# Optimization experiments

Hardware: AMD Instinct MI355X
Metric: run time of the kernel (lower is better)

The kernel has to match this reference:

```python
import jax, jax.numpy as jnp
import numpy as np

B, T, C, H = 4, 1024, 1024, 16
HD = C // H
EPS = 1e-5


def _layernorm(x, w, b):
    mu = jnp.mean(x, axis=-1, keepdims=True)
    var = jnp.mean(jnp.square(x - mu), axis=-1, keepdims=True)
    return (x - mu) * jax.lax.rsqrt(var + EPS) * w + b


def setup_inputs() -> dict:
    key = jax.random.key(0)
    ks = jax.random.split(key, 10)
    s = 0.02
    return {
        "x": jax.random.normal(ks[0], (B, T, C), jnp.float32),
        "attention_mask": jnp.zeros((1, 1, T, T), jnp.float32),
        "ln1_w": jnp.ones((C,), jnp.float32),
        "ln1_b": jnp.zeros((C,), jnp.float32),
        "w_qkv": s * jax.random.normal(ks[1], (3 * C, C), jnp.float32),
        "b_qkv": jnp.zeros((3 * C,), jnp.float32),
        "w_o": s * jax.random.normal(ks[2], (C, C), jnp.float32),
        "b_o": jnp.zeros((C,), jnp.float32),
        "ln2_w": jnp.ones((C,), jnp.float32),
        "ln2_b": jnp.zeros((C,), jnp.float32),
        "w_fc": s * jax.random.normal(ks[3], (4 * C, C), jnp.float32),
        "b_fc": jnp.zeros((4 * C,), jnp.float32),
        "w_proj": s * jax.random.normal(ks[4], (C, 4 * C), jnp.float32),
        "b_proj": jnp.zeros((C,), jnp.float32),
    }


def reference(x, attention_mask, ln1_w, ln1_b, w_qkv, b_qkv, w_o, b_o,
              ln2_w, ln2_b, w_fc, b_fc, w_proj, b_proj):
    # --- self-attention on ln_1(x) ---
    h = _layernorm(x, ln1_w, ln1_b)
    qkv = h @ w_qkv.T + b_qkv                      # [B,T,3C]
    q, k, v = jnp.split(qkv, 3, axis=-1)
    q = q.reshape(B, T, H, HD).transpose(0, 2, 1, 3)  # [B,H,T,HD]
    k = k.reshape(B, T, H, HD).transpose(0, 2, 1, 3)
    v = v.reshape(B, T, H, HD).transpose(0, 2, 1, 3)
    att = jnp.einsum('bhqd,bhkd->bhqk', q, k) * (1.0 / np.sqrt(HD))
    att = att + attention_mask
    att_weights = jax.nn.softmax(att, axis=-1)     # [B,H,T,T]
    y = jnp.einsum('bhqk,bhkd->bhqd', att_weights, v)
    y = y.transpose(0, 2, 1, 3).reshape(B, T, C)
    y = y @ w_o.T + b_o
    x = x + y
    # --- MLP on ln_2(x), residual ---
    residual = x
    h2 = _layernorm(x, ln2_w, ln2_b)
    h2 = jax.nn.gelu(h2 @ w_fc.T + b_fc, approximate=False)
    h2 = h2 @ w_proj.T + b_proj
    x = residual + h2
    return (x, att_weights)
```

## Files before the change

kernel.cpp:

```cpp
#include <hip/hip_runtime.h>
#include <stdint.h>
#include <math.h>

typedef __attribute__((ext_vector_type(4))) float f32x4;
typedef __attribute__((ext_vector_type(8))) short s16x8;
typedef __attribute__((ext_vector_type(4))) unsigned short u16x4;
typedef __attribute__((ext_vector_type(8))) unsigned short u16x8;

__device__ __forceinline__ unsigned short f2b(float x) {
    union { float f; uint32_t u; } v; v.f = x;
    uint32_t r = v.u + 0x7FFFu + ((v.u >> 16) & 1u);
    return (unsigned short)(r >> 16);
}
__device__ __forceinline__ float b2f(unsigned short u) {
    union { uint32_t u; float f; } v; v.u = (uint32_t)u << 16;
    return v.f;
}

__device__ __forceinline__ void gload16(const unsigned short* g, unsigned short* l) {
    __builtin_amdgcn_global_load_lds(
        (const __attribute__((address_space(1))) unsigned int*)(const void*)g,
        (__attribute__((address_space(3))) unsigned int*)(void*)l,
        16, 0, 0);
}

__global__ __launch_bounds__(256) void cast4_kernel(
        const float* __restrict__ a, int na, const float* __restrict__ b, int nb,
        const float* __restrict__ c, int nc, const float* __restrict__ d, int nd,
        unsigned short* __restrict__ oa, unsigned short* __restrict__ ob,
        unsigned short* __restrict__ oc, unsigned short* __restrict__ od) {
    int i = blockIdx.x * 256 + threadIdx.x;
    const float* src; unsigned short* dst; int off;
    if (i < na)                { src = a; dst = oa; off = i; }
    else if (i < na+nb)        { src = b; dst = ob; off = i - na; }
    else if (i < na+nb+nc)     { src = c; dst = oc; off = i - na - nb; }
    else if (i < na+nb+nc+nd)  { src = d; dst = od; off = i - na - nb - nc; }
    else return;
    f32x4 v = ((const f32x4*)src)[off];
    u16x4 o;
    #pragma unroll
    for (int j = 0; j < 4; ++j) o[j] = f2b(v[j]);
    ((u16x4*)dst)[off] = o;
}

__global__ __launch_bounds__(256) void ln_kernel(const float* __restrict__ x,
                                                 const float* __restrict__ w,
                                                 const float* __restrict__ b,
                                                 unsigned short* __restrict__ out) {
    const long row = blockIdx.x;
    const int tid = threadIdx.x;
    f32x4 v = *(const f32x4*)(x + row * 1024 + tid * 4);
    float s  = v[0] + v[1] + v[2] + v[3];
    float sq = v[0]*v[0] + v[1]*v[1] + v[2]*v[2] + v[3]*v[3];
    #pragma unroll
    for (int off = 32; off; off >>= 1) {
        s  += __shfl_xor(s, off);
        sq += __shfl_xor(sq, off);
    }
    __shared__ float red[8];
    if ((tid & 63) == 0) { red[tid >> 6] = s; red[4 + (tid >> 6)] = sq; }
    __syncthreads();
    s  = red[0] + red[1] + red[2] + red[3];
    sq = red[4] + red[5] + red[6] + red[7];
    float mu  = s * (1.0f / 1024.0f);
    float var = sq * (1.0f / 1024.0f) - mu * mu;
    float rs  = rsqrtf(var + 1e-5f);
    f32x4 wv = *(const f32x4*)(w + tid * 4);
    f32x4 bv = *(const f32x4*)(b + tid * 4);
    u16x4 o;
    #pragma unroll
    for (int j = 0; j < 4; ++j) o[j] = f2b((v[j] - mu) * rs * wv[j] + bv[j]);
    *(u16x4*)(out + row * 1024 + tid * 4) = o;
}

__global__ __launch_bounds__(256) void inv_kernel(const float* __restrict__ psum,
                                                  float* __restrict__ invl) {
    const long r = blockIdx.x * 256 + threadIdx.x;
    const float* p = psum + (r << 4);
    f32x4 a = *(const f32x4*)p,       b = *(const f32x4*)(p + 4);
    f32x4 c = *(const f32x4*)(p + 8), d = *(const f32x4*)(p + 12);
    float s = (a[0]+a[1]+a[2]+a[3]) + (b[0]+b[1]+b[2]+b[3])
            + (c[0]+c[1]+c[2]+c[3]) + (d[0]+d[1]+d[2]+d[3]);
    invl[r] = 1.0f / s;
}

__global__ __launch_bounds__(256)
void pv_att(const unsigned short* __restrict__ E,
            const unsigned short* __restrict__ Vt,
            const float* __restrict__ invl,
            float* __restrict__ att,
            unsigned short* __restrict__ y) {
    __shared__ unsigned short ldsA[3][64 * 32];
    __shared__ unsigned short ldsB[3][64 * 32];
    const int tid = threadIdx.x, lane = tid & 63, wid = tid >> 6;
    const int wr = wid >> 1, wc = wid & 1;
    const int bh = blockIdx.y;
    const int q0 = blockIdx.x * 64;
    const int fr = lane & 15, fs = lane >> 4;

    const unsigned short* Ab = E + ((long)bh << 20) + (long)q0 * 1024;
    const unsigned short* Bb = Vt + ((long)bh << 16);

    const int e0  = wid * 512 + lane * 8;
    const int r0a = e0 >> 5, c0a = e0 & 31;
    const float il_a = invl[(bh << 10) + q0 + r0a];
    float* attRow = att + ((long)bh << 20) + (long)(q0 + r0a) * 1024 + c0a;

    f32x4 acc[2][2] = {};

#define PSTAGE(T, BUF)                                                        \
    {                                                                         \
        const int k0s = (T) << 5;                                             \
        gload16(Ab + k0s + (long)r0a * 1024 + c0a, &ldsA[BUF][wid * 512]);    \
        gload16(Bb + k0s + (long)r0a * 1024 + c0a, &ldsB[BUF][wid * 512]);    \
    }

    PSTAGE(0, 0);
    PSTAGE(1, 1);

    for (int t = 0; t < 32; ++t) {
        const int buf = t % 3;
        asm volatile("s_waitcnt vmcnt(4)" ::: "memory");
        __syncthreads();
        if (t + 2 < 32) PSTAGE(t + 2, (t + 2) % 3);

        {
            s16x8 ea = *(const s16x8*)&ldsA[buf][e0];
            f32x4 o0, o1;
            #pragma unroll
            for (int j = 0; j < 4; ++j) o0[j] = b2f((unsigned short)ea[j]) * il_a;
            #pragma unroll
            for (int j = 0; j < 4; ++j) o1[j] = b2f((unsigned short)ea[4 + j]) * il_a;
            *(f32x4*)(attRow + t * 32)     = o0;
            *(f32x4*)(attRow + t * 32 + 4) = o1;
        }

        s16x8 af[2], vb[2];
        #pragma unroll
        for (int m = 0; m < 2; ++m)
            af[m] = *(const s16x8*)&ldsA[buf][(wr * 32 + m * 16 + fr) * 32 + fs * 8];
        #pragma unroll
        for (int n = 0; n < 2; ++n)
            vb[n] = *(const s16x8*)&ldsB[buf][(wc * 32 + n * 16 + fr) * 32 + fs * 8];
        #pragma unroll
        for (int m = 0; m < 2; ++m)
            #pragma unroll
            for (int n = 0; n < 2; ++n)
                acc[m][n] = __builtin_amdgcn_mfma_f32_16x16x32_bf16(af[m], vb[n], acc[m][n], 0, 0, 0);
    }
#undef PSTAGE

    const int bb = bh >> 4, hh = bh & 15;
    #pragma unroll
    for (int m = 0; m < 2; ++m) {
        #pragma unroll
        for (int r = 0; r < 4; ++r) {
            const int trow = q0 + wr * 32 + m * 16 + fs * 4 + r;
            const float il = invl[(bh << 10) + trow];
            #pragma unroll
            for (int n = 0; n < 2; ++n) {
                const int c = hh * 64 + wc * 32 + n * 16 + fr;
                y[((long)(bb * 1024 + trow) << 10) + c] = f2b(acc[m][n][r] * il);
            }
        }
    }
}

template <int BM, int BN, int EPI>
__global__ __launch_bounds__(256)
void gemm_bt(const unsigned short* __restrict__ A,
             const unsigned short* __restrict__ Bm,
             int K, int lda, int ldb, int ldc,
             long sAz, long sBz,
             const float* __restrict__ bias,
             const float* __restrict__ resid,
             float* __restrict__ outF,
             unsigned short* __restrict__ outB) {
    constexpr int WM = BM / 2, WN = BN / 2;
    constexpr int FM = WM / 16, FN = WN / 16;
    constexpr int NTA = BM / 64, NTB = BN / 64;
    constexpr int LOADS = NTA + NTB;
    __shared__ unsigned short ldsA[3][BM * 32];
    __shared__ unsigned short ldsB[3][BN * 32];

    const int tid  = threadIdx.x;
    const int lane = tid & 63;
    const int wid  = tid >> 6;
    const int wr   = wid >> 1, wc = wid & 1;
    const int bz   = blockIdx.z;
    const int row0 = blockIdx.x * BM;
    const int col0 = blockIdx.y * BN;

    const unsigned short* Ab = A + (long)bz * sAz + (long)row0 * lda;
    const unsigned short* Bb = Bm + (long)bz * sBz + (long)col0 * ldb;

    const int nt = K >> 5;
    f32x4 acc[FM][FN] = {};
    const int fr = lane & 15;
    const int fk = (lane >> 4) * 8;

#define STAGE(T, BUF)                                                              \
    {                                                                              \
        const int k0s = (T) << 5;                                                  \
        _Pragma("unroll")                                                          \
        for (int i = 0; i < NTA; ++i) {                                            \
            int e = i * 2048 + wid * 512 + lane * 8;                               \
            gload16(Ab + k0s + (long)(e >> 5) * lda + (e & 31),                    \
                    &ldsA[BUF][i * 2048 + wid * 512]);                             \
        }                                                                          \
        _Pragma("unroll")                                                          \
        for (int i = 0; i < NTB; ++i) {                                            \
            int e = i * 2048 + wid * 512 + lane * 8;                               \
            gload16(Bb + k0s + (long)(e >> 5) * ldb + (e & 31),                    \
                    &ldsB[BUF][i * 2048 + wid * 512]);                             \
        }                                                                          \
    }

    STAGE(0, 0);
    if (nt > 1) STAGE(1, 1);

    for (int t = 0; t < nt; ++t) {
        const int buf = t % 3;
        if (t + 1 < nt) {
            if constexpr (LOADS == 2)      asm volatile("s_waitcnt vmcnt(2)" ::: "memory");
            else if constexpr (LOADS == 3) asm volatile("s_waitcnt vmcnt(3)" ::: "memory");
            else                           asm volatile("s_waitcnt vmcnt(4)" ::: "memory");
        } else {
            asm volatile("s_waitcnt vmcnt(0)" ::: "memory");
        }
        __syncthreads();
        if (t + 2 < nt) STAGE(t + 2, (t + 2) % 3);

        s16x8 af[FM], bfr[FN];
        #pragma unroll
        for (int m = 0; m < FM; ++m)
            af[m] = *(const s16x8*)&ldsA[buf][(wr * WM + m * 16 + fr) * 32 + fk];
        #pragma unroll
        for (int n = 0; n < FN; ++n)
            bfr[n] = *(const s16x8*)&ldsB[buf][(wc * WN + n * 16 + fr) * 32 + fk];
        #pragma unroll
        for (int m = 0; m < FM; ++m)
            #pragma unroll
            for (int n = 0; n < FN; ++n)
                acc[m][n] = __builtin_amdgcn_mfma_f32_16x16x32_bf16(af[m], bfr[n], acc[m][n], 0, 0, 0);
    }
#undef STAGE

    const int cj = lane & 15;
    const int r0 = (lane >> 4) * 4;

    if constexpr (EPI == 1) {
        #pragma unroll
        for (int m = 0; m < FM; ++m) {
            #pragma unroll
            for (int r = 0; r < 4; ++r) {
                const int grow = row0 + wr * WM + m * 16 + r0 + r;
                float rs = 0.0f;
                #pragma unroll
                for (int n = 0; n < FN; ++n) {
                    const int gcol = col0 + wc * WN + n * 16 + cj;
                    float e = __expf(acc[m][n][r] + resid[((long)grow << 10) + gcol]);
                    rs += e;
                    outB[((long)bz << 20) + ((long)grow << 10) + gcol] = f2b(e);
                }
                rs += __shfl_xor(rs, 1); rs += __shfl_xor(rs, 2);
                rs += __shfl_xor(rs, 4); rs += __shfl_xor(rs, 8);
                if (cj == 0)
                    outF[((((long)bz << 10) + grow) << 4) + blockIdx.y * 2 + wc] = rs;
            }
        }
    } else {
        #pragma unroll
        for (int m = 0; m < FM; ++m) {
            #pragma unroll
            for (int n = 0; n < FN; ++n) {
                #pragma unroll
                for (int r = 0; r < 4; ++r) {
                    const int grow = row0 + wr * WM + m * 16 + r0 + r;
                    const int gcol = col0 + wc * WN + n * 16 + cj;
                    float v = acc[m][n][r];
                    if constexpr (EPI == 0) {
                        v += bias[gcol];
                        const int bb = grow >> 10, t = grow & 1023;
                        const int seg = gcol >> 10, mm = gcol & 1023;
                        const int hh = mm >> 6, dd = mm & 63;
                        const long bh = bb * 16 + hh;
                        if (seg == 0)
                            outB[(bh << 16) + (t << 6) + dd] = f2b(v * 0.125f);
                        else if (seg == 1)
                            outB[4194304 + (bh << 16) + (t << 6) + dd] = f2b(v);
                        else
                            outB[8388608 + (bh << 16) + (dd << 10) + t] = f2b(v);
                    } else if constexpr (EPI == 3) {
                        const long idx = ((long)grow << 10) + gcol;
                        outF[idx] = v + bias[gcol] + resid[idx];
                    } else if constexpr (EPI == 4) {
                        float u = v + bias[gcol];
                        float g = 0.5f * u * (1.0f + erff(u * 0.70710678118f));
                        outB[(long)grow * ldc + gcol] = f2b(g);
                    }
                }
            }
        }
    }
}

extern "C" void kernel_launch(void* const* d_in, const int* in_sizes, int n_in,
                              void* d_out, int out_size, void* d_ws, size_t ws_size,
                              hipStream_t stream) {
    (void)in_sizes; (void)n_in; (void)out_size; (void)ws_size;
    const float* x     = (const float*)d_in[0];
    const float* mask  = (const float*)d_in[1];
    const float* ln1w  = (const float*)d_in[2];
    const float* ln1b  = (const float*)d_in[3];
    const float* wqkv  = (const float*)d_in[4];
    const float* bqkv  = (const float*)d_in[5];
    const float* wo    = (const float*)d_in[6];
    const float* bo    = (const float*)d_in[7];
    const float* ln2w  = (const float*)d_in[8];
    const float* ln2b  = (const float*)d_in[9];
    const float* wfc   = (const float*)d_in[10];
    const float* bfc   = (const float*)d_in[11];
    const float* wproj = (const float*)d_in[12];
    const float* bproj = (const float*)d_in[13];

    float* outx = (float*)d_out;
    float* att  = (float*)d_out + 4194304;

    char* ws = (char*)d_ws;
    unsigned short* h_bf     = (unsigned short*)ws;  ws += (size_t)8  << 20;
    unsigned short* wqkv_bf  = (unsigned short*)ws;  ws += (size_t)6  << 20;
    unsigned short* wo_bf    = (unsigned short*)ws;  ws += (size_t)2  << 20;
    unsigned short* wfc_bf   = (unsigned short*)ws;  ws += (size_t)8  << 20;
    unsigned short* wproj_bf = (unsigned short*)ws;  ws += (size_t)8  << 20;
    unsigned short* q_bf     = (unsigned short*)ws;  ws += (size_t)24 << 20;
    unsigned short* k_bf     = q_bf + 4194304;
    unsigned short* vT_bf    = q_bf + 8388608;
    unsigned short* e_b      = (unsigned short*)ws;  ws += (size_t)128 << 20;
    unsigned short* y_bf     = (unsigned short*)ws;  ws += (size_t)8  << 20;
    float*          x2       = (float*)ws;           ws += (size_t)16 << 20;
    unsigned short* gelu_bf  = (unsigned short*)ws;  ws += (size_t)32 << 20;
    float*          psum     = (float*)ws;           ws += (size_t)4  << 20;
    float*          invl     = (float*)ws;           ws += (size_t)256 << 10;

    cast4_kernel<<<12288, 256, 0, stream>>>(
        wqkv, 786432, wo, 262144, wfc, 1048576, wproj, 1048576,
        wqkv_bf, wo_bf, wfc_bf, wproj_bf);

    ln_kernel<<<4096, 256, 0, stream>>>(x, ln1w, ln1b, h_bf);

    gemm_bt<128, 128, 0><<<dim3(32, 24, 1), 256, 0, stream>>>(
        h_bf, wqkv_bf, 1024, 1024, 1024, 0, 0, 0,
        bqkv, nullptr, nullptr, q_bf);

    gemm_bt<128, 128, 1><<<dim3(8, 8, 64), 256, 0, stream>>>(
        q_bf, k_bf, 64, 64, 64, 0, 65536, 65536,
        nullptr, mask, psum, e_b);

    inv_kernel<<<256, 256, 0, stream>>>(psum, invl);

    pv_att<<<dim3(16, 64), 256, 0, stream>>>(e_b, vT_bf, invl, att, y_bf);

    gemm_bt<64, 128, 3><<<dim3(64, 8, 1), 256, 0, stream>>>(
        y_bf, wo_bf, 1024, 1024, 1024, 1024, 0, 0,
        bo, x, x2, nullptr);

    ln_kernel<<<4096, 256, 0, stream>>>(x2, ln2w, ln2b, h_bf);

    gemm_bt<128, 128, 4><<<dim3(32, 32, 1), 256, 0, stream>>>(
        h_bf, wfc_bf, 1024, 1024, 1024, 4096, 0, 0,
        bfc, nullptr, nullptr, gelu_bf);

    gemm_bt<64, 128, 3><<<dim3(64, 8, 1), 256, 0, stream>>>(
        gelu_bf, wproj_bf, 4096, 4096, 4096, 1024, 0, 0,
        bproj, x2, outx, nullptr);
}
```

Baseline: 448.9 us.

## Add 256x256 tile GEMM with 8 waves for QKV and FC projections

Introduces a new gemm256 kernel with 512 threads, 256x256 output tiles, XOR-swizzled LDS reads, a triple-buffered global-to-LDS prefetch interleaved across four compute phases, and s_setprio around the MFMA bursts. The QKV and FC GEMMs move to it, while gemm_bt is reduced to the residual epilogue. Larger tiles raise arithmetic intensity and cut global and LDS traffic per FLOP. The cost is that QKV launches only 192 blocks and FC only 256 on a 256-CU part, which may underfill the device, and the extra barriers per K step add synchronisation.

```diff
diff --git a/kernel.cpp b/kernel.cpp
--- a/kernel.cpp
+++ b/kernel.cpp
@@ -5,7 +5,6 @@
 typedef __attribute__((ext_vector_type(4))) float f32x4;
 typedef __attribute__((ext_vector_type(8))) short s16x8;
 typedef __attribute__((ext_vector_type(4))) unsigned short u16x4;
-typedef __attribute__((ext_vector_type(8))) unsigned short u16x8;
 
 __device__ __forceinline__ unsigned short f2b(float x) {
     union { float f; uint32_t u; } v; v.f = x;
@@ -22,6 +21,10 @@
         (const __attribute__((address_space(1))) unsigned int*)(const void*)g,
         (__attribute__((address_space(3))) unsigned int*)(void*)l,
         16, 0, 0);
+}
+
+__device__ __forceinline__ s16x8 rdsw(const unsigned short* t, int row, int kg) {
+    return *(const s16x8*)(t + row * 32 + ((kg ^ ((row >> 2) & 3)) << 3));
 }
 
 __global__ __launch_bounds__(256) void cast4_kernel(
@@ -166,6 +169,114 @@
     }
 }
 
+template <int EPI>
+__global__ __launch_bounds__(512, 2)
+void gemm256(const unsigned short* __restrict__ A,
+             const unsigned short* __restrict__ Bm,
+             int K, int lda, int ldb, int ldc,
+             const float* __restrict__ bias,
+             unsigned short* __restrict__ outB) {
+    __shared__ unsigned short ldsA[3 * 8192];
+    __shared__ unsigned short ldsB[3 * 8192];
+    const int tid = threadIdx.x, lane = tid & 63, wid = tid >> 6;
+    const int wr = wid >> 2, wcn = wid & 3;
+    const int fr = lane & 15, kg = lane >> 4;
+    const int row0 = blockIdx.x * 256, col0 = blockIdx.y * 256;
+    const unsigned short* Ab = A + (long)row0 * lda;
+    const unsigned short* Bb = Bm + (long)col0 * ldb;
+    const int nt = K >> 5;
+
+    const int srow = tid >> 2;
+    const int schk = (tid & 3) ^ ((tid >> 4) & 3);
+    const long aoff  = (long)srow * lda + schk * 8;
+    const long boff  = (long)srow * ldb + schk * 8;
+    const long aoff2 = aoff + (long)128 * lda;
+    const long boff2 = boff + (long)128 * ldb;
+
+#define PA0(T) gload16(Ab + ((long)(T) << 5) + aoff,  ldsA + ((T) % 3) * 8192        + wid * 64 * 8)
+#define PA1(T) gload16(Ab + ((long)(T) << 5) + aoff2, ldsA + ((T) % 3) * 8192 + 4096 + wid * 64 * 8)
+#define PB0(T) gload16(Bb + ((long)(T) << 5) + boff,  ldsB + ((T) % 3) * 8192        + wid * 64 * 8)
+#define PB1(T) gload16(Bb + ((long)(T) << 5) + boff2, ldsB + ((T) % 3) * 8192 + 4096 + wid * 64 * 8)
+
+    PA0(0); PA1(0); PB0(0); PB1(0);
+    PA0(1); PA1(1); PB0(1); PB1(1);
+
+    f32x4 acc[8][4] = {};
+
+#define PHASE(Q, PF)                                                                   \
+    {                                                                                  \
+        s16x8 aA = rdsw(As, wr * 128 + (Q) * 32 + fr, kg);                             \
+        s16x8 aB = rdsw(As, wr * 128 + (Q) * 32 + 16 + fr, kg);                        \
+        PF;                                                                            \
+        __builtin_amdgcn_s_setprio(1);                                                 \
+        _Pragma("unroll")                                                              \
+        for (int n = 0; n < 4; ++n)                                                    \
+            acc[2*(Q)][n] = __builtin_amdgcn_mfma_f32_16x16x32_bf16(aA, bb[n], acc[2*(Q)][n], 0, 0, 0); \
+        _Pragma("unroll")                                                              \
+        for (int n = 0; n < 4; ++n)                                                    \
+            acc[2*(Q)+1][n] = __builtin_amdgcn_mfma_f32_16x16x32_bf16(aB, bb[n], acc[2*(Q)+1][n], 0, 0, 0); \
+        __builtin_amdgcn_s_setprio(0);                                                 \
+    }
+
+    for (int t = 0; t < nt; ++t) {
+        const unsigned short* As = ldsA + (t % 3) * 8192;
+        const unsigned short* Bs = ldsB + (t % 3) * 8192;
+        if (t + 1 < nt) asm volatile("s_waitcnt vmcnt(4)" ::: "memory");
+        else            asm volatile("s_waitcnt vmcnt(0)" ::: "memory");
+        __syncthreads();
+
+        s16x8 bb[4];
+        #pragma unroll
+        for (int n = 0; n < 4; ++n)
+            bb[n] = rdsw(Bs, wcn * 64 + n * 16 + fr, kg);
+        const bool pf = (t + 2 < nt);
+
+        PHASE(0, if (pf) PA0(t + 2));
+        __syncthreads();
+        PHASE(1, if (pf) PA1(t + 2));
+        __syncthreads();
+        PHASE(2, if (pf) PB0(t + 2));
+        __syncthreads();
+        PHASE(3, if (pf) PB1(t + 2));
+    }
+#undef PHASE
+#undef PA0
+#undef PA1
+#undef PB0
+#undef PB1
+
+    const int cj = fr, r0q = kg * 4;
+    #pragma unroll
+    for (int m = 0; m < 8; ++m) {
+        #pragma unroll
+        for (int n = 0; n < 4; ++n) {
+            #pragma unroll
+            for (int r = 0; r < 4; ++r) {
+                const int grow = row0 + wr * 128 + m * 16 + r0q + r;
+                const int gcol = col0 + wcn * 64 + n * 16 + cj;
+                float v = acc[m][n][r];
+                if constexpr (EPI == 0) {
+                    v += bias[gcol];
+                    const int bbv = grow >> 10, tt = grow & 1023;
+                    const int seg = gcol >> 10, mm = gcol & 1023;
+                    const int hh = mm >> 6, dd = mm & 63;
+                    const long bh = bbv * 16 + hh;
+                    if (seg == 0)
+                        outB[(bh << 16) + (tt << 6) + dd] = f2b(v * 0.125f);
+                    else if (seg == 1)
+                        outB[4194304 + (bh << 16) + (tt << 6) + dd] = f2b(v);
+                    else
+                        outB[8388608 + (bh << 16) + (dd << 10) + tt] = f2b(v);
+                } else if constexpr (EPI == 4) {
+                    float u = v + bias[gcol];
+                    float g = 0.5f * u * (1.0f + erff(u * 0.70710678118f));
+                    outB[(long)grow * ldc + gcol] = f2b(g);
+                }
+            }
+        }
+    }
+}
+
 template <int BM, int BN, int EPI>
 __global__ __launch_bounds__(256)
 void gemm_bt(const unsigned short* __restrict__ A,
@@ -279,26 +390,8 @@
                     const int grow = row0 + wr * WM + m * 16 + r0 + r;
                     const int gcol = col0 + wc * WN + n * 16 + cj;
                     float v = acc[m][n][r];
-                    if constexpr (EPI == 0) {
-                        v += bias[gcol];
-                        const int bb = grow >> 10, t = grow & 1023;
-                        const int seg = gcol >> 10, mm = gcol & 1023;
-                        const int hh = mm >> 6, dd = mm & 63;
-                        const long bh = bb * 16 + hh;
-                        if (seg == 0)
-                            outB[(bh << 16) + (t << 6) + dd] = f2b(v * 0.125f);
-                        else if (seg == 1)
-                            outB[4194304 + (bh << 16) + (t << 6) + dd] = f2b(v);
-                        else
-                            outB[8388608 + (bh << 16) + (dd << 10) + t] = f2b(v);
-                    } else if constexpr (EPI == 3) {
-                        const long idx = ((long)grow << 10) + gcol;
-                        outF[idx] = v + bias[gcol] + resid[idx];
-                    } else if constexpr (EPI == 4) {
-                        float u = v + bias[gcol];
-                        float g = 0.5f * u * (1.0f + erff(u * 0.70710678118f));
-                        outB[(long)grow * ldc + gcol] = f2b(g);
-                    }
+                    const long idx = ((long)grow << 10) + gcol;
+                    outF[idx] = v + bias[gcol] + resid[idx];
                 }
             }
         }
@@ -349,9 +442,8 @@
 
     ln_kernel<<<4096, 256, 0, stream>>>(x, ln1w, ln1b, h_bf);
 
-    gemm_bt<128, 128, 0><<<dim3(32, 24, 1), 256, 0, stream>>>(
-        h_bf, wqkv_bf, 1024, 1024, 1024, 0, 0, 0,
-        bqkv, nullptr, nullptr, q_bf);
+    gemm256<0><<<dim3(16, 12), 512, 0, stream>>>(
+        h_bf, wqkv_bf, 1024, 1024, 1024, 0, bqkv, q_bf);
 
     gemm_bt<128, 128, 1><<<dim3(8, 8, 64), 256, 0, stream>>>(
         q_bf, k_bf, 64, 64, 64, 0, 65536, 65536,
@@ -367,9 +459,8 @@
 
     ln_kernel<<<4096, 256, 0, stream>>>(x2, ln2w, ln2b, h_bf);
 
-    gemm_bt<128, 128, 4><<<dim3(32, 32, 1), 256, 0, stream>>>(
-        h_bf, wfc_bf, 1024, 1024, 1024, 4096, 0, 0,
-        bfc, nullptr, nullptr, gelu_bf);
+    gemm256<4><<<dim3(16, 16), 512, 0, stream>>>(
+        h_bf, wfc_bf, 1024, 1024, 1024, 4096, bfc, gelu_bf);
 
     gemm_bt<64, 128, 3><<<dim3(64, 8, 1), 256, 0, stream>>>(
         gelu_bf, wproj_bf, 4096, 4096, 4096, 1024, 0, 0,
```

After: 481.2 us. 7.2% more time.

## Add 256x256 tile GEMM for QKV/FC and XCD-aware block swizzle

Applied to the files above, without the earlier changes.

Adds a new 512-thread GEMM kernel with 256x256 output tiles and double-buffered LDS, used for the QKV projection and the FC+GELU GEMM. The larger tiles raise arithmetic intensity and cut redundant global loads. Block indices are remapped so consecutive tiles land on the same XCD, which should improve L2 reuse, and the remap is also applied to the output and proj GEMMs. The trade-off is fewer blocks (192/256) for 256 CUs and higher register pressure, which may leave some CUs idle on the QKV GEMM.

```diff
diff --git a/kernel.cpp b/kernel.cpp
--- a/kernel.cpp
+++ b/kernel.cpp
@@ -5,7 +5,6 @@
 typedef __attribute__((ext_vector_type(4))) float f32x4;
 typedef __attribute__((ext_vector_type(8))) short s16x8;
 typedef __attribute__((ext_vector_type(4))) unsigned short u16x4;
-typedef __attribute__((ext_vector_type(8))) unsigned short u16x8;
 
 __device__ __forceinline__ unsigned short f2b(float x) {
     union { float f; uint32_t u; } v; v.f = x;
@@ -166,11 +165,107 @@
     }
 }
 
-template <int BM, int BN, int EPI>
+template <int EPI>
+__global__ __launch_bounds__(512, 2)
+void gemm256(const unsigned short* __restrict__ A,
+             const unsigned short* __restrict__ Bm,
+             int K, int lda, int ldb, int ldc, int nx,
+             const float* __restrict__ bias,
+             unsigned short* __restrict__ outB) {
+    __shared__ unsigned short ldsA[2][8192];
+    __shared__ unsigned short ldsB[2][8192];
+    const int tid = threadIdx.x, lane = tid & 63, wid = tid >> 6;
+    const int wr = wid >> 2, wcn = wid & 3;
+    const int fr = lane & 15, kg = lane >> 4;
+
+    const int nwg = gridDim.x, q = nwg >> 3, n = blockIdx.x;
+    const int m0 = (n & 7) * q + (n >> 3);
+    const int bx = m0 % nx, by = m0 / nx;
+    const int row0 = bx * 256, col0 = by * 256;
+
+    const unsigned short* Ab = A + (long)row0 * lda;
+    const unsigned short* Bb = Bm + (long)col0 * ldb;
+    const int nt = K >> 5;
+
+    const int e0 = tid * 8, e1 = 4096 + tid * 8;
+    const int ra0 = e0 >> 5, ca0 = e0 & 31;
+    const int ra1 = e1 >> 5, ca1 = e1 & 31;
+
+#define STAGE(T, BUF)                                                         \
+    {                                                                         \
+        const int k0s = (T) << 5;                                             \
+        gload16(Ab + k0s + (long)ra0 * lda + ca0, &ldsA[BUF][e0 & ~7]);       \
+        gload16(Ab + k0s + (long)ra1 * lda + ca1, &ldsA[BUF][e1 & ~7]);       \
+        gload16(Bb + k0s + (long)ra0 * ldb + ca0, &ldsB[BUF][e0 & ~7]);       \
+        gload16(Bb + k0s + (long)ra1 * ldb + ca1, &ldsB[BUF][e1 & ~7]);       \
+    }
+
+    STAGE(0, 0);
+
+    f32x4 acc[8][4] = {};
+    for (int t = 0; t < nt; ++t) {
+        const int buf = t & 1;
+        if (t + 1 < nt) {
+            STAGE(t + 1, buf ^ 1);
+            asm volatile("s_waitcnt vmcnt(4)" ::: "memory");
+        } else {
+            asm volatile("s_waitcnt vmcnt(0)" ::: "memory");
+        }
+        __syncthreads();
+
+        s16x8 af[8], bb[4];
+        #pragma unroll
+        for (int m = 0; m < 8; ++m)
+            af[m] = *(const s16x8*)&ldsA[buf][(wr * 128 + m * 16 + fr) * 32 + kg * 8];
+        #pragma unroll
+        for (int nn = 0; nn < 4; ++nn)
+            bb[nn] = *(const s16x8*)&ldsB[buf][(wcn * 64 + nn * 16 + fr) * 32 + kg * 8];
+        #pragma unroll
+        for (int m = 0; m < 8; ++m)
+            #pragma unroll
+            for (int nn = 0; nn < 4; ++nn)
+                acc[m][nn] = __builtin_amdgcn_mfma_f32_16x16x32_bf16(af[m], bb[nn], acc[m][nn], 0, 0, 0);
+        __syncthreads();
+    }
+#undef STAGE
+
+    const int cj = fr, r0q = kg * 4;
+    #pragma unroll
+    for (int m = 0; m < 8; ++m) {
+        #pragma unroll
+        for (int nn = 0; nn < 4; ++nn) {
+            #pragma unroll
+            for (int r = 0; r < 4; ++r) {
+                const int grow = row0 + wr * 128 + m * 16 + r0q + r;
+                const int gcol = col0 + wcn * 64 + nn * 16 + cj;
+                float v = acc[m][nn][r];
+                if constexpr (EPI == 0) {
+                    v += bias[gcol];
+                    const int bbv = grow >> 10, tt = grow & 1023;
+                    const int seg = gcol >> 10, mm = gcol & 1023;
+                    const int hh = mm >> 6, dd = mm & 63;
+                    const long bh = bbv * 16 + hh;
+                    if (seg == 0)
+                        outB[(bh << 16) + (tt << 6) + dd] = f2b(v * 0.125f);
+                    else if (seg == 1)
+                        outB[4194304 + (bh << 16) + (tt << 6) + dd] = f2b(v);
+                    else
+                        outB[8388608 + (bh << 16) + (dd << 10) + tt] = f2b(v);
+                } else if constexpr (EPI == 4) {
+                    float u = v + bias[gcol];
+                    float g = 0.5f * u * (1.0f + erff(u * 0.70710678118f));
+                    outB[(long)grow * ldc + gcol] = f2b(g);
+                }
+            }
+        }
+    }
+}
+
+template <int BM, int BN, int EPI, bool SWZ>
 __global__ __launch_bounds__(256)
 void gemm_bt(const unsigned short* __restrict__ A,
              const unsigned short* __restrict__ Bm,
-             int K, int lda, int ldb, int ldc,
+             int K, int lda, int ldb, int ldc, int nx,
              long sAz, long sBz,
              const float* __restrict__ bias,
              const float* __restrict__ resid,
@@ -188,8 +283,17 @@
     const int wid  = tid >> 6;
     const int wr   = wid >> 1, wc = wid & 1;
     const int bz   = blockIdx.z;
-    const int row0 = blockIdx.x * BM;
-    const int col0 = blockIdx.y * BN;
+
+    int bx, by;
+    if constexpr (SWZ) {
+        const int nwg = gridDim.x, q = nwg >> 3, n = blockIdx.x;
+        const int m0 = (n & 7) * q + (n >> 3);
+        bx = m0 % nx; by = m0 / nx;
+    } else {
+        bx = blockIdx.x; by = blockIdx.y;
+    }
+    const int row0 = bx * BM;
+    const int col0 = by * BN;
 
     const unsigned short* Ab = A + (long)bz * sAz + (long)row0 * lda;
     const unsigned short* Bb = Bm + (long)bz * sBz + (long)col0 * ldb;
@@ -266,7 +370,7 @@
                 rs += __shfl_xor(rs, 1); rs += __shfl_xor(rs, 2);
                 rs += __shfl_xor(rs, 4); rs += __shfl_xor(rs, 8);
                 if (cj == 0)
-                    outF[((((long)bz << 10) + grow) << 4) + blockIdx.y * 2 + wc] = rs;
+                    outF[((((long)bz << 10) + grow) << 4) + by * 2 + wc] = rs;
             }
         }
     } else {
@@ -279,26 +383,8 @@
                     const int grow = row0 + wr * WM + m * 16 + r0 + r;
                     const int gcol = col0 + wc * WN + n * 16 + cj;
                     float v = acc[m][n][r];
-                    if constexpr (EPI == 0) {
-                        v += bias[gcol];
-                        const int bb = grow >> 10, t = grow & 1023;
-                        const int seg = gcol >> 10, mm = gcol & 1023;
-                        const int hh = mm >> 6, dd = mm & 63;
-                        const long bh = bb * 16 + hh;
-                        if (seg == 0)
-                            outB[(bh << 16) + (t << 6) + dd] = f2b(v * 0.125f);
-                        else if (seg == 1)
-                            outB[4194304 + (bh << 16) + (t << 6) + dd] = f2b(v);
-                        else
-                            outB[8388608 + (bh << 16) + (dd << 10) + t] = f2b(v);
-                    } else if constexpr (EPI == 3) {
-                        const long idx = ((long)grow << 10) + gcol;
-                        outF[idx] = v + bias[gcol] + resid[idx];
-                    } else if constexpr (EPI == 4) {
-                        float u = v + bias[gcol];
-                        float g = 0.5f * u * (1.0f + erff(u * 0.70710678118f));
-                        outB[(long)grow * ldc + gcol] = f2b(g);
-                    }
+                    const long idx = ((long)grow << 10) + gcol;
+                    outF[idx] = v + bias[gcol] + resid[idx];
                 }
             }
         }
@@ -349,29 +435,27 @@
 
     ln_kernel<<<4096, 256, 0, stream>>>(x, ln1w, ln1b, h_bf);
 
-    gemm_bt<128, 128, 0><<<dim3(32, 24, 1), 256, 0, stream>>>(
-        h_bf, wqkv_bf, 1024, 1024, 1024, 0, 0, 0,
-        bqkv, nullptr, nullptr, q_bf);
-
-    gemm_bt<128, 128, 1><<<dim3(8, 8, 64), 256, 0, stream>>>(
-        q_bf, k_bf, 64, 64, 64, 0, 65536, 65536,
+    gemm256<0><<<192, 512, 0, stream>>>(
+        h_bf, wqkv_bf, 1024, 1024, 1024, 0, 16, bqkv, q_bf);
+
+    gemm_bt<128, 128, 1, false><<<dim3(8, 8, 64), 256, 0, stream>>>(
+        q_bf, k_bf, 64, 64, 64, 0, 8, 65536, 65536,
         nullptr, mask, psum, e_b);
 
     inv_kernel<<<256, 256, 0, stream>>>(psum, invl);
 
     pv_att<<<dim3(16, 64), 256, 0, stream>>>(e_b, vT_bf, invl, att, y_bf);
 
-    gemm_bt<64, 128, 3><<<dim3(64, 8, 1), 256, 0, stream>>>(
-        y_bf, wo_bf, 1024, 1024, 1024, 1024, 0, 0,
+    gemm_bt<64, 128, 3, true><<<512, 256, 0, stream>>>(
+        y_bf, wo_bf, 1024, 1024, 1024, 1024, 64, 0, 0,
         bo, x, x2, nullptr);
 
     ln_kernel<<<4096, 256, 0, stream>>>(x2, ln2w, ln2b, h_bf);
 
-    gemm_bt<128, 128, 4><<<dim3(32, 32, 1), 256, 0, stream>>>(
-        h_bf, wfc_bf, 1024, 1024, 1024, 4096, 0, 0,
-        bfc, nullptr, nullptr, gelu_bf);
-
-    gemm_bt<64, 128, 3><<<dim3(64, 8, 1), 256, 0, stream>>>(
-        gelu_bf, wproj_bf, 4096, 4096, 4096, 1024, 0, 0,
+    gemm256<4><<<256, 512, 0, stream>>>(
+        h_bf, wfc_bf, 1024, 1024, 1024, 4096, 16, bfc, gelu_bf);
+
+    gemm_bt<64, 128, 3, true><<<512, 256, 0, stream>>>(
+        gelu_bf, wproj_bf, 4096, 4096, 4096, 1024, 64, 0, 0,
         bproj, x2, outx, nullptr);
 }
```

Result: slower. 488.6 us (+8.8%).
